# Optimization experiments

Hardware: AMD Instinct MI355X
Metric: run time of the kernel (lower is better)

## Reference

```python
import jax, jax.numpy as jnp
import numpy as np

D = 1024      # neural_dim
M = 8192      # memory_size (assumed fully used)
H = 16        # num_heads
B = 64        # batch
HD = D // H   # head dim


def setup_inputs() -> dict:
    key = jax.random.key(0)
    ks = jax.random.split(key, 24)
    s = 0.02
    inp = {
        "neural_input": jax.random.normal(ks[0], (B, D), jnp.float32),
        "memory_keys": jax.random.normal(ks[1], (M, D), jnp.float32),
        "memory_values": jax.random.normal(ks[2], (M, D), jnp.float32),
        # query/key/value projections (nn.Linear weights are [out, in])
        "Wq": jax.random.normal(ks[3], (D, D), jnp.float32) * s,
        "bq": jnp.zeros((D,), jnp.float32),
        "Wk": jax.random.normal(ks[4], (D, D), jnp.float32) * s,
        "bk": jnp.zeros((D,), jnp.float32),
        "Wv": jax.random.normal(ks[5], (D, D), jnp.float32) * s,
        "bv": jnp.zeros((D,), jnp.float32),
        # MultiheadAttention packed in-projection [3D, D] and out projection
        "in_proj_w": jax.random.normal(ks[6], (3 * D, D), jnp.float32) * s,
        "in_proj_b": jnp.zeros((3 * D,), jnp.float32),
        "out_w": jax.random.normal(ks[7], (D, D), jnp.float32) * s,
        "out_b": jnp.zeros((D,), jnp.float32),
        # memory_gate: Linear(2D->D), ReLU, Linear(D->D), Sigmoid
        "gW1": jax.random.normal(ks[8], (D, 2 * D), jnp.float32) * s,
        "gb1": jnp.zeros((D,), jnp.float32),
        "gW2": jax.random.normal(ks[9], (D, D), jnp.float32) * s,
        "gb2": jnp.zeros((D,), jnp.float32),
        # integration: Linear(2D->2D), ReLU, Linear(2D->D)
        "iW1": jax.random.normal(ks[10], (2 * D, 2 * D), jnp.float32) * s,
        "ib1": jnp.zeros((2 * D,), jnp.float32),
        "iW2": jax.random.normal(ks[11], (D, 2 * D), jnp.float32) * s,
        "ib2": jnp.zeros((D,), jnp.float32),
    }
    return inp


def reference(neural_input, memory_keys, memory_values,
              Wq, bq, Wk, bk, Wv, bv,
              in_proj_w, in_proj_b, out_w, out_b,
              gW1, gb1, gW2, gb2, iW1, ib1, iW2, ib2):
    x = neural_input  # [B, D]
    # pre-projections (memory_used assumed all True -> full tables)
    q = x @ Wq.T + bq                  # [B, D]
    k = memory_keys @ Wk.T + bk        # [M, D]
    v = memory_values @ Wv.T + bv      # [M, D]

    # MultiheadAttention (single query per batch element; K/V shared
    # across batch instead of the redundant expand in the original)
    Wiq, Wik, Wiv = in_proj_w[:D], in_proj_w[D:2 * D], in_proj_w[2 * D:]
    biq, bik, biv = in_proj_b[:D], in_proj_b[D:2 * D], in_proj_b[2 * D:]
    qh = (q @ Wiq.T + biq).reshape(B, H, HD)   # [B, H, hd]
    kh = (k @ Wik.T + bik).reshape(M, H, HD)   # [M, H, hd]
    vh = (v @ Wiv.T + biv).reshape(M, H, HD)   # [M, H, hd]

    scale = 1.0 / np.sqrt(HD).astype(np.float32)
    scores = jnp.einsum('bhd,mhd->bhm', qh, kh) * scale  # [B, H, M]
    attn = jax.nn.softmax(scores, axis=-1)
    ctx = jnp.einsum('bhm,mhd->bhd', attn, vh).reshape(B, D)
    memory_signal = ctx @ out_w.T + out_b      # [B, D]

    # gated fusion
    gate_in = jnp.concatenate([x, memory_signal], axis=-1)          # [B, 2D]
    gate = jax.nn.sigmoid(jax.nn.relu(gate_in @ gW1.T + gb1) @ gW2.T + gb2)
    gated_memory = gate * memory_signal
    combined = jnp.concatenate([x, gated_memory], axis=-1)          # [B, 2D]
    out = jax.nn.relu(combined @ iW1.T + ib1) @ iW2.T + ib2         # [B, D]
    return out
```

## Files before the change

kernel.cpp:

```cpp
#include <hip/hip_runtime.h>
#include <hip/hip_bf16.h>
#include <stdint.h>


typedef __bf16 bf16;
typedef __bf16 bf16x4 __attribute__((ext_vector_type(4)));
typedef __bf16 bf16x8 __attribute__((ext_vector_type(8)));
typedef float f32x4 __attribute__((ext_vector_type(4)));

#define D_ 1024
#define M_ 8192
#define B_ 64
#define H_ 16

static __device__ __forceinline__ void gload16(const void* g, void* l) {
  __builtin_amdgcn_global_load_lds(
      (const __attribute__((address_space(1))) void*)g,
      (__attribute__((address_space(3))) void*)l, 16, 0, 0);
}

static __device__ __forceinline__ f32x4 mfma16(bf16x8 a, bf16x8 b, f32x4 c) {
  return __builtin_amdgcn_mfma_f32_16x16x32_bf16(a, b, c, 0, 0, 0);
}

template <int U, int KLEN, typename OutT>
__device__ __forceinline__ void thin_gemm(
    const bf16* __restrict__ A, int lda,
    const bf16* __restrict__ Bm, int ldb,
    OutT* __restrict__ C, int ldc,
    const float* __restrict__ bias, float scale) {
  const int tid = threadIdx.x, lane = tid & 63, w = tid >> 6;
  const int rl = lane & 15, qq = lane >> 4;
  const bf16* pa = A + (int64_t)(w * 16 + rl) * lda + qq * 8;
  const bf16* pb[4];
  pb[0] = Bm + (int64_t)rl * ldb + qq * 8;
  pb[1] = pb[0] + (int64_t)16 * ldb;
  pb[2] = pb[0] + (int64_t)32 * ldb;
  pb[3] = pb[0] + (int64_t)48 * ldb;
  f32x4 acc[4] = {};
  bf16x8 av[2][U], bv[2][U][4];
#pragma unroll
  for (int u = 0; u < U; u++) {
    av[0][u] = *(const bf16x8*)(pa + u * 32);
#pragma unroll
    for (int j = 0; j < 4; j++)
      bv[0][u][j] = *(const bf16x8*)(pb[j] + u * 32);
  }
  constexpr int NI = KLEN / (32 * U);
#pragma unroll
  for (int it = 0; it < NI; it++) {
    const int cur = it & 1, nxt = cur ^ 1;
    if (it + 1 < NI) {
      int k = (it + 1) * 32 * U;
#pragma unroll
      for (int u = 0; u < U; u++) {
        av[nxt][u] = *(const bf16x8*)(pa + k + u * 32);
#pragma unroll
        for (int j = 0; j < 4; j++)
          bv[nxt][u][j] = *(const bf16x8*)(pb[j] + k + u * 32);
      }
    }
#pragma unroll
    for (int u = 0; u < U; u++)
#pragma unroll
      for (int j = 0; j < 4; j++)
        acc[j] = mfma16(av[cur][u], bv[cur][u][j], acc[j]);
  }
#pragma unroll
  for (int j = 0; j < 4; j++) {
    int gn = j * 16 + rl;
    float bb = bias ? bias[gn] : 0.0f;
#pragma unroll
    for (int r = 0; r < 4; r++) {
      int gm = w * 16 + qq * 4 + r;
      C[(int64_t)gm * ldc + gn] = (OutT)((acc[j][r] + bb) * scale);
    }
  }
}

struct CvtD { const float* src; bf16* dst; int end; };
struct PrepArgs {
  CvtD d[9];
  const float *Wq, *Wk, *Wv, *inw, *inb, *bq, *bk, *bv;
  const float *outb, *gb1, *gb2, *ib1, *ib2;
  bf16* WT;
  float *bc, *msR, *g1R, *gateR, *h1R, *out, *Oraw, *lmat;
};

__global__ __launch_bounds__(256) void prep_kernel(PrepArgs a) {
  const int bx = blockIdx.x, tid = threadIdx.x;
  if (bx < 29760) {
    int g = bx * 256 + tid;
    CvtD dd = a.d[8];
    int begin = a.d[7].end;
#pragma unroll
    for (int t = 7; t >= 0; t--)
      if (g < a.d[t].end) { dd = a.d[t]; begin = t ? a.d[t - 1].end : 0; }
    int i = (g - begin) * 4;
    float4 v = *(const float4*)(dd.src + i);
    bf16x4 o = { (bf16)v.x, (bf16)v.y, (bf16)v.z, (bf16)v.w };
    *(bf16x4*)(dd.dst + i) = o;
  } else if (bx < 32832) {
    int t = bx - 29760;
    int z = t >> 10, rem = t & 1023;
    const float* src = z == 0 ? a.Wq : z == 1 ? a.Wk : a.Wv;
    bf16* out = a.WT + (int64_t)z * D_ * D_;
    __shared__ bf16 tile[32][33];
    int tx = tid & 31, ty = tid >> 5;
    int r0 = (rem >> 5) * 32, c0 = (rem & 31) * 32;
#pragma unroll
    for (int i = 0; i < 32; i += 8)
      tile[ty + i][tx] = (bf16)src[(int64_t)(r0 + ty + i) * D_ + c0 + tx];
    __syncthreads();
#pragma unroll
    for (int i = 0; i < 32; i += 8)
      out[(int64_t)(c0 + ty + i) * D_ + r0 + tx] = tile[tx][ty + i];
  } else if (bx < 33600) {
    int t = bx - 32832;
    int w = tid >> 6, lane = tid & 63;
    int ng = t * 4 + w;
    int z = ng >> 10;
    const float* Wi = a.inw + (int64_t)ng * D_;
    const float* b = z == 0 ? a.bq : z == 1 ? a.bk : a.bv;
    float acc = 0.f;
#pragma unroll
    for (int l = 0; l < D_; l += 64) acc += Wi[l + lane] * b[l + lane];
#pragma unroll
    for (int m = 32; m; m >>= 1) acc += __shfl_xor(acc, m, 64);
    if (lane == 0) a.bc[ng] = acc + a.inb[ng];
  } else if (bx < 33984) {
    int t = bx - 33600;
    int seg = t >> 6, row = t & 63;
    int n = tid * 4;
    const float* b;
    float* dst;
    int bn = n;
    if (seg == 0)      { dst = a.msR   + row * 1024;        b = a.outb; }
    else if (seg == 1) { dst = a.g1R   + row * 1024;        b = a.gb1;  }
    else if (seg == 2) { dst = a.gateR + row * 1024;        b = a.gb2;  }
    else if (seg == 3) { dst = a.h1R   + row * 2048;        b = a.ib1;  }
    else if (seg == 4) { dst = a.h1R   + row * 2048 + 1024; b = a.ib1; bn = 1024 + n; }
    else               { dst = a.out   + row * 1024;        b = a.ib2;  }
    *(float4*)(dst + n) = *(const float4*)(b + bn);
  } else {
    int b = bx - 33984;
    float4 z4 = {0.f, 0.f, 0.f, 0.f};
    *(float4*)(a.Oraw + b * 1024 + tid * 4) = z4;
    if (b < 16 && tid < 64) a.lmat[b * 64 + tid] = 0.f;
  }
}

template <int MODE>
__global__ __launch_bounds__(256) void gemm_big(
    const bf16* __restrict__ A, int lda, int64_t sA,
    const bf16* __restrict__ Bm, int ldb, int64_t sB,
    bf16* __restrict__ C, int ldc, int64_t sC, bf16* __restrict__ Ct,
    const float* __restrict__ bias, int64_t sbias, int K,
    const bf16* __restrict__ qA, const bf16* __restrict__ qB,
    bf16* __restrict__ qC, const float* __restrict__ qbias) {
  int m0, n0, z;
  if (MODE == 0) {
    z = blockIdx.z; m0 = blockIdx.y * 128; n0 = blockIdx.x * 128;
  } else {
    if ((int)blockIdx.x >= 1024) {
      int n0q = ((int)blockIdx.x - 1024) * 64;
      thin_gemm<2, 1024, bf16>(qA, D_, qB + (int64_t)n0q * D_, D_,
                               qC + n0q, D_, qbias + n0q, 0.125f);
      return;
    }
    int lin = blockIdx.x, xcd = lin & 7, slot = lin >> 3;
    z = slot >> 6;
    int r = slot & 63;
    m0 = (xcd * 8 + (r >> 3)) * 128;
    n0 = (r & 7) * 128;
  }
  A += (int64_t)z * sA; Bm += (int64_t)z * sB;
  if (bias) bias += (int64_t)z * sbias;
  __shared__ alignas(16) bf16 As[128 * 32];
  __shared__ alignas(16) bf16 Bs[128 * 32];
  const int tid = threadIdx.x, lane = tid & 63, w = tid >> 6;
  const int wm = (w & 1) * 64, wn = (w >> 1) * 64;
  const int rl = lane & 15, qq = lane >> 4;
  f32x4 acc[4][4] = {};

  int c0 = w * 64 + lane, c1 = (4 + w) * 64 + lane;
  int ra0 = c0 >> 2, qa0 = (c0 & 3) ^ ((ra0 >> 1) & 3);
  int ra1 = c1 >> 2, qa1 = (c1 & 3) ^ ((ra1 >> 1) & 3);
  const bf16* gA0 = A + (int64_t)(m0 + ra0) * lda + qa0 * 8;
  const bf16* gA1 = A + (int64_t)(m0 + ra1) * lda + qa1 * 8;
  const bf16* gB0 = Bm + (int64_t)(n0 + ra0) * ldb + qa0 * 8;
  const bf16* gB1 = Bm + (int64_t)(n0 + ra1) * ldb + qa1 * 8;
  bf16* lA0 = As + w * 512;
  bf16* lA1 = As + (4 + w) * 512;
  bf16* lB0 = Bs + w * 512;
  bf16* lB1 = Bs + (4 + w) * 512;

  for (int k0 = 0; k0 < K; k0 += 32) {
    __syncthreads();
    gload16(gA0 + k0, lA0);
    gload16(gA1 + k0, lA1);
    gload16(gB0 + k0, lB0);
    gload16(gB1 + k0, lB1);
    __syncthreads();
    bf16x8 af[4], bb[4];
#pragma unroll
    for (int i = 0; i < 4; i++) {
      int r = wm + i * 16 + rl;
      af[i] = *(const bf16x8*)(As + r * 32 + (qq ^ ((r >> 1) & 3)) * 8);
    }
#pragma unroll
    for (int j = 0; j < 4; j++) {
      int r = wn + j * 16 + rl;
      bb[j] = *(const bf16x8*)(Bs + r * 32 + (qq ^ ((r >> 1) & 3)) * 8);
    }
#pragma unroll
    for (int i = 0; i < 4; i++)
#pragma unroll
      for (int j = 0; j < 4; j++)
        acc[i][j] = mfma16(af[i], bb[j], acc[i][j]);
  }
  if (MODE == 1 && z == 1) {
#pragma unroll
    for (int j = 0; j < 4; j++) {
      int gn = n0 + wn + j * 16 + rl;
      float bb2 = bias ? bias[gn] : 0.0f;
#pragma unroll
      for (int i = 0; i < 4; i++) {
        int gm0 = m0 + wm + i * 16 + qq * 4;
        f32x4 a = acc[i][j];
        bf16x4 o = { (bf16)(a[0] + bb2), (bf16)(a[1] + bb2),
                     (bf16)(a[2] + bb2), (bf16)(a[3] + bb2) };
        *(bf16x4*)(Ct + (int64_t)gn * M_ + gm0) = o;
      }
    }
  } else {
    C += (int64_t)z * sC;
#pragma unroll
    for (int j = 0; j < 4; j++) {
      int gn = n0 + wn + j * 16 + rl;
      float bb2 = bias ? bias[gn] : 0.0f;
#pragma unroll
      for (int i = 0; i < 4; i++) {
        int gm0 = m0 + wm + i * 16 + qq * 4;
#pragma unroll
        for (int r = 0; r < 4; r++)
          C[(int64_t)(gm0 + r) * ldc + gn] = (bf16)(acc[i][j][r] + bb2);
      }
    }
  }
}

__global__ __launch_bounds__(512) void gemm256(
    const bf16* __restrict__ A,
    const bf16* __restrict__ Wc,
    const float* __restrict__ bc,
    bf16* __restrict__ kh, bf16* __restrict__ vhT,
    const bf16* __restrict__ qA, const bf16* __restrict__ qB,
    bf16* __restrict__ qC, const float* __restrict__ qbias) {
  extern __shared__ __align__(16) bf16 lds[];
  const int bid = blockIdx.x;
  if (bid >= 256) {
    if (threadIdx.x < 256) {
      int n0q = (bid - 256) * 64;
      thin_gemm<2, 1024, bf16>(qA, D_, qB + (int64_t)n0q * D_, D_,
                               qC + n0q, D_, qbias + n0q, 0.125f);
    }
    return;
  }
  const int lin = bid;
  const int xcd = lin & 7, s = lin >> 3;
  const int z = xcd >> 2;
  const int m0 = ((xcd & 3) * 8 + (s >> 2)) * 256;
  const int n0 = (s & 3) * 256;
  const bf16* Ab = A + (int64_t)z * M_ * D_;
  const bf16* Bb = Wc + (int64_t)(z + 1) * D_ * D_;
  const float* bias = bc + (z + 1) * D_;

  const int tid = threadIdx.x, lane = tid & 63, w = tid >> 6;
  const int rl = lane & 15, qq = lane >> 4;
  const int wr = w >> 2, wcn = w & 3;

  const int ci0 = w * 128 + lane, ci1 = ci0 + 64;
  const int ra0 = ci0 >> 2, ca0 = (ci0 & 3) ^ ((ra0 >> 1) & 3);
  const int ra1 = ci1 >> 2, ca1 = (ci1 & 3) ^ ((ra1 >> 1) & 3);
  const bf16* gA0 = Ab + (int64_t)(m0 + ra0) * D_ + ca0 * 8;
  const bf16* gA1 = Ab + (int64_t)(m0 + ra1) * D_ + ca1 * 8;
  const bf16* gB0 = Bb + (int64_t)(n0 + ra0) * D_ + ca0 * 8;
  const bf16* gB1 = Bb + (int64_t)(n0 + ra1) * D_ + ca1 * 8;
  const int lA0 = w * 1024, lA1 = lA0 + 512;

#define STAGE3(kt)                                   \
  do {                                               \
    bf16* bse = lds + ((kt) & 3) * 16384;            \
    int ko = (kt) * 32;                              \
    gload16(gA0 + ko, bse + lA0);                    \
    gload16(gA1 + ko, bse + lA1);                    \
    gload16(gB0 + ko, bse + 8192 + lA0);             \
    gload16(gB1 + ko, bse + 8192 + lA1);             \
  } while (0)
#define FENCE3 asm volatile("" ::: "memory")
#define BARRIER3                       \
  do {                                 \
    FENCE3;                            \
    __builtin_amdgcn_s_barrier();      \
    FENCE3;                            \
  } while (0)

  f32x4 acc[8][4] = {};
  const int sq8 = (qq ^ ((rl >> 1) & 3)) * 8;

  auto compute = [&](int kt) {
    const bf16* ba = lds + (kt & 3) * 16384;
    const bf16* bbp = ba + 8192;
    bf16x8 bfr[4], afr[8];
#pragma unroll
    for (int j = 0; j < 4; j++)
      bfr[j] = *(const bf16x8*)(bbp + (wcn * 64 + j * 16 + rl) * 32 + sq8);
#pragma unroll
    for (int mi = 0; mi < 8; mi++)
      afr[mi] = *(const bf16x8*)(ba + (wr * 128 + mi * 16 + rl) * 32 + sq8);
    __builtin_amdgcn_s_setprio(1);
#pragma unroll
    for (int mi = 0; mi < 8; mi++)
#pragma unroll
      for (int j = 0; j < 4; j++)
        acc[mi][j] = mfma16(afr[mi], bfr[j], acc[mi][j]);
    __builtin_amdgcn_s_setprio(0);
  };

  constexpr int NT = 32;
  STAGE3(0);
  STAGE3(1);
  STAGE3(2);
#pragma unroll 1
  for (int kt = 0; kt < NT - 2; kt++) {
    asm volatile("s_waitcnt vmcnt(8)" ::: "memory");
    BARRIER3;
    if (kt + 3 < NT) STAGE3(kt + 3);
    compute(kt);
  }
  asm volatile("s_waitcnt vmcnt(4)" ::: "memory");
  BARRIER3;
  compute(NT - 2);
  asm volatile("s_waitcnt vmcnt(0)" ::: "memory");
  BARRIER3;
  compute(NT - 1);

  if (z == 0) {
#pragma unroll
    for (int j = 0; j < 4; j++) {
      int gn = n0 + wcn * 64 + j * 16 + rl;
      float bb2 = bias[gn];
#pragma unroll
      for (int mi = 0; mi < 8; mi++) {
        int gm0 = m0 + wr * 128 + mi * 16 + qq * 4;
#pragma unroll
        for (int r = 0; r < 4; r++)
          kh[(int64_t)(gm0 + r) * D_ + gn] = (bf16)(acc[mi][j][r] + bb2);
      }
    }
  } else {
#pragma unroll
    for (int j = 0; j < 4; j++) {
      int gn = n0 + wcn * 64 + j * 16 + rl;
      float bb2 = bias[gn];
#pragma unroll
      for (int mi = 0; mi < 8; mi++) {
        int gm0 = m0 + wr * 128 + mi * 16 + qq * 4;
        f32x4 a = acc[mi][j];
        bf16x4 o = { (bf16)(a[0] + bb2), (bf16)(a[1] + bb2),
                     (bf16)(a[2] + bb2), (bf16)(a[3] + bb2) };
        *(bf16x4*)(vhT + (int64_t)gn * M_ + gm0) = o;
      }
    }
  }
#undef STAGE3
#undef FENCE3
#undef BARRIER3
}

__global__ __launch_bounds__(256, 2) void flash_kernel(
    const bf16* __restrict__ qh, const bf16* __restrict__ kh,
    const bf16* __restrict__ vhT, float* __restrict__ Oraw,
    float* __restrict__ lmat) {
  const int tid = threadIdx.x, lane = tid & 63, w = tid >> 6;
  const int rl = lane & 15, qq = lane >> 4;
  const int h = blockIdx.x >> 4, c = blockIdx.x & 15;
  __shared__ alignas(16) bf16 Plds[4 * 16 * 72];
  const bf16* qhp = qh + (int64_t)(w * 16 + rl) * D_ + h * 64 + qq * 8;
  bf16x8 aq0 = *(const bf16x8*)(qhp);
  bf16x8 aq1 = *(const bf16x8*)(qhp + 32);
  float lsum[4] = {0.f, 0.f, 0.f, 0.f};
  f32x4 acc_o[4] = {};
  bf16* pl = Plds + w * 1152;
  const bf16* khb = kh + (int64_t)(c * 512) * D_ + h * 64 + qq * 8;
  const bf16* vtb = vhT + (int64_t)(h * 64) * M_ + c * 512 + qq * 8;
  for (int nt = 0; nt < 8; nt++) {
    int mb = nt * 64;
    bf16x8 bk0[4], bk1[4], vv0[4], vv1[4];
#pragma unroll
    for (int j = 0; j < 4; j++) {
      const bf16* p = khb + (int64_t)(mb + j * 16 + rl) * D_;
      bk0[j] = *(const bf16x8*)(p);
      bk1[j] = *(const bf16x8*)(p + 32);
      const bf16* q = vtb + (int64_t)(j * 16 + rl) * M_ + mb;
      vv0[j] = *(const bf16x8*)(q);
      vv1[j] = *(const bf16x8*)(q + 32);
    }
    f32x4 s[4] = {};
#pragma unroll
    for (int j = 0; j < 4; j++) {
      s[j] = mfma16(aq0, bk0[j], s[j]);
      s[j] = mfma16(aq1, bk1[j], s[j]);
    }
#pragma unroll
    for (int j = 0; j < 4; j++)
#pragma unroll
      for (int r = 0; r < 4; r++) {
        float p = __expf(s[j][r]);
        lsum[r] += p;
        pl[(qq * 4 + r) * 72 + j * 16 + rl] = (bf16)p;
      }
    bf16x8 pa0 = *(const bf16x8*)(pl + rl * 72 + qq * 8);
    bf16x8 pa1 = *(const bf16x8*)(pl + rl * 72 + 32 + qq * 8);
#pragma unroll
    for (int j = 0; j < 4; j++) {
      acc_o[j] = mfma16(pa0, vv0[j], acc_o[j]);
      acc_o[j] = mfma16(pa1, vv1[j], acc_o[j]);
    }
  }
#pragma unroll
  for (int msk = 1; msk <= 8; msk <<= 1)
#pragma unroll
    for (int r = 0; r < 4; r++) lsum[r] += __shfl_xor(lsum[r], msk, 64);
#pragma unroll
  for (int j = 0; j < 4; j++)
#pragma unroll
    for (int r = 0; r < 4; r++)
      atomicAdd(&Oraw[(int64_t)(w * 16 + qq * 4 + r) * D_ + h * 64 + j * 16 + rl],
                acc_o[j][r]);
  if (rl == 0)
#pragma unroll
    for (int r = 0; r < 4; r++)
      atomicAdd(&lmat[h * 64 + w * 16 + qq * 4 + r], lsum[r]);
}

struct Chunk { const void* p0; const void* p1; int ld; int kind; };
struct StageArgs { Chunk c[16]; };

template <int NKK>
__global__ __launch_bounds__(256) void tail_stage(
    StageArgs sa, const bf16* __restrict__ Bw, int ldb,
    float* __restrict__ Craw, int ldc) {
  const int n0 = blockIdx.x * 64, kc = blockIdx.y;
  const int bk0 = kc * NKK * 32;
  const Chunk ch = sa.c[kc];
  const int tid = threadIdx.x, lane = tid & 63, w = tid >> 6;
  const int rl = lane & 15, qq = lane >> 4;
  const int m = w * 16 + rl;
  const bf16* pb[4];
#pragma unroll
  for (int j = 0; j < 4; j++)
    pb[j] = Bw + (int64_t)(n0 + j * 16 + rl) * ldb + bk0 + qq * 8;
  f32x4 acc[4] = {};
#pragma unroll
  for (int kk = 0; kk < NKK; kk++) {
    bf16x8 af;
    if (ch.kind == 0) {
      af = *(const bf16x8*)((const bf16*)ch.p0 + (int64_t)m * ch.ld +
                            kk * 32 + qq * 8);
    } else {
      const float* p = (const float*)ch.p0 + (int64_t)m * ch.ld + kk * 32 + qq * 8;
      float4 u0 = *(const float4*)p;
      float4 u1 = *(const float4*)(p + 4);
      if (ch.kind == 2) {
        u0.x = fmaxf(u0.x, 0.f); u0.y = fmaxf(u0.y, 0.f);
        u0.z = fmaxf(u0.z, 0.f); u0.w = fmaxf(u0.w, 0.f);
        u1.x = fmaxf(u1.x, 0.f); u1.y = fmaxf(u1.y, 0.f);
        u1.z = fmaxf(u1.z, 0.f); u1.w = fmaxf(u1.w, 0.f);
      } else if (ch.kind == 3) {
        const float* pm = (const float*)ch.p1 + (int64_t)m * ch.ld + kk * 32 + qq * 8;
        float4 m0 = *(const float4*)pm;
        float4 m1 = *(const float4*)(pm + 4);
        u0.x = m0.x / (1.f + __expf(-u0.x)); u0.y = m0.y / (1.f + __expf(-u0.y));
        u0.z = m0.z / (1.f + __expf(-u0.z)); u0.w = m0.w / (1.f + __expf(-u0.w));
        u1.x = m1.x / (1.f + __expf(-u1.x)); u1.y = m1.y / (1.f + __expf(-u1.y));
        u1.z = m1.z / (1.f + __expf(-u1.z)); u1.w = m1.w / (1.f + __expf(-u1.w));
      } else if (ch.kind == 4) {
        int hidx = (bk0 + kk * 32) >> 6;
        float linv = 1.0f / ((const float*)ch.p1)[hidx * 64 + m];
        u0.x *= linv; u0.y *= linv; u0.z *= linv; u0.w *= linv;
        u1.x *= linv; u1.y *= linv; u1.z *= linv; u1.w *= linv;
      }
      af = (bf16x8){ (bf16)u0.x, (bf16)u0.y, (bf16)u0.z, (bf16)u0.w,
                     (bf16)u1.x, (bf16)u1.y, (bf16)u1.z, (bf16)u1.w };
    }
    bf16x8 bf_[4];
#pragma unroll
    for (int j = 0; j < 4; j++) bf_[j] = *(const bf16x8*)(pb[j] + kk * 32);
#pragma unroll
    for (int j = 0; j < 4; j++) acc[j] = mfma16(af, bf_[j], acc[j]);
  }
#pragma unroll
  for (int j = 0; j < 4; j++) {
    int gn = n0 + j * 16 + rl;
#pragma unroll
    for (int r = 0; r < 4; r++) {
      int gm = w * 16 + qq * 4 + r;
      atomicAdd(&Craw[(int64_t)gm * ldc + gn], acc[j][r]);
    }
  }
}

extern "C" void kernel_launch(void* const* d_in, const int* in_sizes, int n_in,
                              void* d_out, int out_size, void* d_ws,
                              size_t ws_size, hipStream_t stream) {
  (void)in_sizes; (void)n_in; (void)out_size;
  const float* x    = (const float*)d_in[0];
  const float* mk   = (const float*)d_in[1];
  const float* mv   = (const float*)d_in[2];
  const float* Wq   = (const float*)d_in[3];
  const float* bq   = (const float*)d_in[4];
  const float* Wk   = (const float*)d_in[5];
  const float* bk   = (const float*)d_in[6];
  const float* Wv   = (const float*)d_in[7];
  const float* bv   = (const float*)d_in[8];
  const float* inw  = (const float*)d_in[9];
  const float* inb  = (const float*)d_in[10];
  const float* outw = (const float*)d_in[11];
  const float* outb = (const float*)d_in[12];
  const float* gW1  = (const float*)d_in[13];
  const float* gb1  = (const float*)d_in[14];
  const float* gW2  = (const float*)d_in[15];
  const float* gb2  = (const float*)d_in[16];
  const float* iW1  = (const float*)d_in[17];
  const float* ib1  = (const float*)d_in[18];
  const float* iW2  = (const float*)d_in[19];
  const float* ib2  = (const float*)d_in[20];

  char* ws = (char*)d_ws;
  size_t off = 0;
  auto alloc = [&](size_t bytes) {
    char* p = ws + off;
    off += (bytes + 255) & ~(size_t)255;
    return p;
  };
  bf16* mkmv  = (bf16*)alloc((size_t)2 * M_ * D_ * 2);
  bf16* inpj  = (bf16*)alloc((size_t)3 * D_ * D_ * 2);
  bf16* WT    = (bf16*)alloc((size_t)3 * D_ * D_ * 2);
  bf16* Wc    = (bf16*)alloc((size_t)3 * D_ * D_ * 2);
  float* bc   = (float*)alloc(3 * D_ * 4);
  bf16* xbf   = (bf16*)alloc((size_t)B_ * D_ * 2);
  bf16* qh    = (bf16*)alloc((size_t)B_ * D_ * 2);
  bf16* kh    = (bf16*)alloc((size_t)M_ * D_ * 2);
  bf16* vhT   = (bf16*)alloc((size_t)M_ * D_ * 2);
  float* Oraw = (float*)alloc((size_t)B_ * D_ * 4);
  float* lmat = (float*)alloc((size_t)H_ * B_ * 4);
  float* msR  = (float*)alloc((size_t)B_ * D_ * 4);
  float* g1R  = (float*)alloc((size_t)B_ * D_ * 4);
  float* gateR= (float*)alloc((size_t)B_ * D_ * 4);
  float* h1R  = (float*)alloc((size_t)B_ * 2 * D_ * 4);
  bf16* gW1b  = (bf16*)alloc((size_t)D_ * 2 * D_ * 2);
  bf16* gW2b  = (bf16*)alloc((size_t)D_ * D_ * 2);
  bf16* iW1b  = (bf16*)alloc((size_t)2 * D_ * 2 * D_ * 2);
  bf16* iW2b  = (bf16*)alloc((size_t)D_ * 2 * D_ * 2);
  bf16* outwb = (bf16*)alloc((size_t)D_ * D_ * 2);
  if (ws_size < off) return;

  PrepArgs pa;
  pa.d[0] = { mk,   mkmv,           2097152 };
  pa.d[1] = { mv,   mkmv + M_ * D_, 4194304 };
  pa.d[2] = { inw,  inpj,           4980736 };
  pa.d[3] = { gW1,  gW1b,           5505024 };
  pa.d[4] = { gW2,  gW2b,           5767168 };
  pa.d[5] = { iW1,  iW1b,           6815744 };
  pa.d[6] = { iW2,  iW2b,           7340032 };
  pa.d[7] = { outw, outwb,          7602176 };
  pa.d[8] = { x,    xbf,            7618560 };
  pa.Wq = Wq; pa.Wk = Wk; pa.Wv = Wv; pa.inw = inw; pa.inb = inb;
  pa.bq = bq; pa.bk = bk; pa.bv = bv;
  pa.outb = outb; pa.gb1 = gb1; pa.gb2 = gb2; pa.ib1 = ib1; pa.ib2 = ib2;
  pa.WT = WT; pa.bc = bc; pa.msR = msR; pa.g1R = g1R; pa.gateR = gateR;
  pa.h1R = h1R; pa.out = (float*)d_out; pa.Oraw = Oraw; pa.lmat = lmat;
  prep_kernel<<<dim3(34048), 256, 0, stream>>>(pa);

  gemm_big<0><<<dim3(8, 8, 3), 256, 0, stream>>>(
      inpj, D_, (int64_t)D_ * D_, WT, D_, (int64_t)D_ * D_,
      Wc, D_, (int64_t)D_ * D_, nullptr, nullptr, 0, D_,
      nullptr, nullptr, nullptr, nullptr);

  hipFuncSetAttribute((const void*)gemm256,
                      hipFuncAttributeMaxDynamicSharedMemorySize, 131072);
  gemm256<<<dim3(272), dim3(512), 131072, stream>>>(
      mkmv, Wc, bc, kh, vhT, xbf, Wc, qh, bc);

  flash_kernel<<<dim3(256), 256, 0, stream>>>(qh, kh, vhT, Oraw, lmat);

  StageArgs s1;
  for (int kc = 0; kc < 8; kc++) s1.c[kc] = { Oraw + kc * 128, lmat, D_, 4 };
  tail_stage<4><<<dim3(16, 8), 256, 0, stream>>>(s1, outwb, D_, msR, D_);

  StageArgs s2;
  for (int kc = 0; kc < 8; kc++)  s2.c[kc] = { xbf + kc * 128, nullptr, D_, 0 };
  for (int kc = 8; kc < 16; kc++) s2.c[kc] = { msR + (kc - 8) * 128, nullptr, D_, 1 };
  tail_stage<4><<<dim3(16, 16), 256, 0, stream>>>(s2, gW1b, 2 * D_, g1R, D_);

  StageArgs s3;
  for (int kc = 0; kc < 8; kc++) s3.c[kc] = { g1R + kc * 128, nullptr, D_, 2 };
  tail_stage<4><<<dim3(16, 8), 256, 0, stream>>>(s3, gW2b, D_, gateR, D_);

  StageArgs s4;
  for (int kc = 0; kc < 8; kc++)  s4.c[kc] = { xbf + kc * 128, nullptr, D_, 0 };
  for (int kc = 8; kc < 16; kc++)
    s4.c[kc] = { gateR + (kc - 8) * 128, msR + (kc - 8) * 128, D_, 3 };
  tail_stage<4><<<dim3(32, 16), 256, 0, stream>>>(s4, iW1b, 2 * D_, h1R, 2 * D_);

  StageArgs s5;
  for (int kc = 0; kc < 16; kc++) s5.c[kc] = { h1R + kc * 128, nullptr, 2 * D_, 2 };
  tail_stage<4><<<dim3(16, 16), 256, 0, stream>>>(s5, iW2b, 2 * D_,
                                                  (float*)d_out, D_);
}
```

Measured before the change: 339.0 us.

## Split K/V projection GEMM main loop into two interleaved half-phases with finer barriers

Restructures the K/V in-projection GEMM main loop so each k-tile is processed in two phases (rows 0-3 then 4-7 of the A fragments). Global-to-LDS loads for the A half and B half of a future tile are issued in separate phases, with sched_barriers and s_barriers around each MFMA cluster. The loop is unrolled by four buffers with explicit vmcnt waits. The aim is to interleave LDS reads, global loads and MFMAs more evenly and lower register pressure by holding only half the A fragments at once. In exchange it adds twice as many workgroup barriers per tile.

```diff
diff --git a/kernel.cpp b/kernel.cpp
--- a/kernel.cpp
+++ b/kernel.cpp
@@ -289,62 +289,91 @@
   const bf16* gB1 = Bb + (int64_t)(n0 + ra1) * D_ + ca1 * 8;
   const int lA0 = w * 1024, lA1 = lA0 + 512;
 
-#define STAGE3(kt)                                   \
+  f32x4 acc[8][4] = {};
+  bf16x8 bfr[4], afr[4];
+  const int sq8 = (qq ^ ((rl >> 1) & 3)) * 8;
+
+#define SCB __builtin_amdgcn_sched_barrier(0)
+#define BARR __builtin_amdgcn_s_barrier()
+#define VMW(N) asm volatile("s_waitcnt vmcnt(" #N ")")
+
+#define STAGE_FULL(BUF, KT)                          \
   do {                                               \
-    bf16* bse = lds + ((kt) & 3) * 16384;            \
-    int ko = (kt) * 32;                              \
-    gload16(gA0 + ko, bse + lA0);                    \
-    gload16(gA1 + ko, bse + lA1);                    \
-    gload16(gB0 + ko, bse + 8192 + lA0);             \
-    gload16(gB1 + ko, bse + 8192 + lA1);             \
+    bf16* bse_ = lds + (BUF) * 16384;                \
+    gload16(gA0 + (KT) * 32, bse_ + lA0);            \
+    gload16(gA1 + (KT) * 32, bse_ + lA1);            \
+    gload16(gB0 + (KT) * 32, bse_ + 8192 + lA0);     \
+    gload16(gB1 + (KT) * 32, bse_ + 8192 + lA1);     \
   } while (0)
-#define FENCE3 asm volatile("" ::: "memory")
-#define BARRIER3                       \
-  do {                                 \
-    FENCE3;                            \
-    __builtin_amdgcn_s_barrier();      \
-    FENCE3;                            \
+
+#define PH_A(BUF, DOSTAGE, SKT)                                              \
+  do {                                                                       \
+    const bf16* ba_ = lds + (BUF) * 16384;                                   \
+    const bf16* bb_ = ba_ + 8192;                                            \
+    for (int j = 0; j < 4; j++)                                              \
+      bfr[j] = *(const bf16x8*)(bb_ + (wcn * 64 + j * 16 + rl) * 32 + sq8);  \
+    for (int mi = 0; mi < 4; mi++)                                           \
+      afr[mi] = *(const bf16x8*)(ba_ + (wr * 128 + mi * 16 + rl) * 32 + sq8);\
+    if (DOSTAGE) {                                                           \
+      bf16* bse_ = lds + ((SKT) & 3) * 16384;                                \
+      gload16(gA0 + (SKT) * 32, bse_ + lA0);                                 \
+      gload16(gA1 + (SKT) * 32, bse_ + lA1);                                 \
+    }                                                                        \
+    SCB; BARR; SCB;                                                          \
+    __builtin_amdgcn_s_setprio(1);                                           \
+    for (int mi = 0; mi < 4; mi++)                                           \
+      for (int j = 0; j < 4; j++)                                            \
+        acc[mi][j] = mfma16(afr[mi], bfr[j], acc[mi][j]);                    \
+    __builtin_amdgcn_s_setprio(0);                                           \
+    SCB; BARR; SCB;                                                          \
   } while (0)
 
-  f32x4 acc[8][4] = {};
-  const int sq8 = (qq ^ ((rl >> 1) & 3)) * 8;
-
-  auto compute = [&](int kt) {
-    const bf16* ba = lds + (kt & 3) * 16384;
-    const bf16* bbp = ba + 8192;
-    bf16x8 bfr[4], afr[8];
-#pragma unroll
-    for (int j = 0; j < 4; j++)
-      bfr[j] = *(const bf16x8*)(bbp + (wcn * 64 + j * 16 + rl) * 32 + sq8);
-#pragma unroll
-    for (int mi = 0; mi < 8; mi++)
-      afr[mi] = *(const bf16x8*)(ba + (wr * 128 + mi * 16 + rl) * 32 + sq8);
-    __builtin_amdgcn_s_setprio(1);
-#pragma unroll
-    for (int mi = 0; mi < 8; mi++)
-#pragma unroll
-      for (int j = 0; j < 4; j++)
-        acc[mi][j] = mfma16(afr[mi], bfr[j], acc[mi][j]);
-    __builtin_amdgcn_s_setprio(0);
-  };
-
-  constexpr int NT = 32;
-  STAGE3(0);
-  STAGE3(1);
-  STAGE3(2);
+#define PH_B(BUF, DOSTAGE, SKT, VMSTMT)                                      \
+  do {                                                                       \
+    const bf16* ba_ = lds + (BUF) * 16384;                                   \
+    for (int mi = 0; mi < 4; mi++)                                           \
+      afr[mi] =                                                              \
+          *(const bf16x8*)(ba_ + (wr * 128 + (mi + 4) * 16 + rl) * 32 + sq8);\
+    if (DOSTAGE) {                                                           \
+      bf16* bse_ = lds + ((SKT) & 3) * 16384;                                \
+      gload16(gB0 + (SKT) * 32, bse_ + 8192 + lA0);                          \
+      gload16(gB1 + (SKT) * 32, bse_ + 8192 + lA1);                          \
+    }                                                                        \
+    VMSTMT;                                                                  \
+    SCB; BARR; SCB;                                                          \
+    __builtin_amdgcn_s_setprio(1);                                           \
+    for (int mi = 0; mi < 4; mi++)                                           \
+      for (int j = 0; j < 4; j++)                                            \
+        acc[mi + 4][j] = mfma16(afr[mi], bfr[j], acc[mi + 4][j]);            \
+    __builtin_amdgcn_s_setprio(0);                                           \
+    SCB; BARR; SCB;                                                          \
+  } while (0)
+
+  STAGE_FULL(0, 0);
+  STAGE_FULL(1, 1);
+  STAGE_FULL(2, 2);
+  VMW(8);
+  SCB; BARR; SCB;
+
 #pragma unroll 1
-  for (int kt = 0; kt < NT - 2; kt++) {
-    asm volatile("s_waitcnt vmcnt(8)" ::: "memory");
-    BARRIER3;
-    if (kt + 3 < NT) STAGE3(kt + 3);
-    compute(kt);
-  }
-  asm volatile("s_waitcnt vmcnt(4)" ::: "memory");
-  BARRIER3;
-  compute(NT - 2);
-  asm volatile("s_waitcnt vmcnt(0)" ::: "memory");
-  BARRIER3;
-  compute(NT - 1);
+  for (int t = 0; t < 7; t++) {
+    const int kb = t * 4;
+    PH_A(0, 1, kb + 3); PH_B(0, 1, kb + 3, VMW(8));
+    PH_A(1, 1, kb + 4); PH_B(1, 1, kb + 4, VMW(8));
+    PH_A(2, 1, kb + 5); PH_B(2, 1, kb + 5, VMW(8));
+    PH_A(3, 1, kb + 6); PH_B(3, 1, kb + 6, VMW(8));
+  }
+  PH_A(0, 1, 31); PH_B(0, 1, 31, VMW(8));
+  PH_A(1, 0, 0);  PH_B(1, 0, 0, VMW(4));
+  PH_A(2, 0, 0);  PH_B(2, 0, 0, VMW(0));
+  PH_A(3, 0, 0);  PH_B(3, 0, 0, (void)0);
+
+#undef SCB
+#undef BARR
+#undef VMW
+#undef STAGE_FULL
+#undef PH_A
+#undef PH_B
 
   if (z == 0) {
 #pragma unroll
@@ -374,9 +403,6 @@
       }
     }
   }
-#undef STAGE3
-#undef FENCE3
-#undef BARRIER3
 }
 
 __global__ __launch_bounds__(256, 2) void flash_kernel(
```

Measured after the change: 343.5 us. No clear change (+1.4%).
